# Kernel optimization log

Hardware: AMD Instinct MI355X
Metric: run time of the kernel (lower is better)

The kernel has to match this reference:

```python
import jax, jax.numpy as jnp
import numpy as np

NUM_NODES = 200000
NUM_EDGES = 500000
B = 4096            # batch size (src, dst, neg each B)
ND = 3 * B          # dst nodes of attention block
K = 10              # sampled neighbors per dst
N = ND * (1 + K)    # total tail nodes
D = 128             # dim_embed == dim_node
DE = 128            # dim_edge
DT = 128            # dim_time
H = 2               # num_heads
DIN = 2 * D + DE + DT  # GRUCell input dim


def time_encode(t, w, b):
    # tglite TimeEncode: cos(t * w + b)
    return jnp.cos(t[..., None] * w + b)


def gru_cell(x, h, w_ih, w_hh, b_ih, b_hh):
    # torch.nn.GRUCell, gate order [r, z, n]
    gi = x @ w_ih.T + b_ih
    gh = h @ w_hh.T + b_hh
    i_r, i_z, i_n = jnp.split(gi, 3, axis=-1)
    h_r, h_z, h_n = jnp.split(gh, 3, axis=-1)
    r = jax.nn.sigmoid(i_r + h_r)
    z = jax.nn.sigmoid(i_z + h_z)
    n = jnp.tanh(i_n + r * h_n)
    return (1.0 - z) * n + z * h


def setup_inputs() -> dict:
    key = jax.random.key(0)
    ks = jax.random.split(key, 40)
    p = lambda i, shape: jax.random.normal(ks[i], shape, dtype=jnp.float32) * 0.05
    return {
        "nodes": jax.random.randint(ks[0], (N,), 0, NUM_NODES),
        "eids": jax.random.randint(ks[1], (ND, K), 0, NUM_EDGES),
        "dt_nbr": jax.random.uniform(ks[2], (ND, K), dtype=jnp.float32) * 1000.0,
        "nfeat": p(3, (NUM_NODES, D)),
        "mem_data": p(4, (NUM_NODES, D)),
        "mem_time": jax.random.uniform(ks[5], (NUM_NODES,), dtype=jnp.float32) * 1000.0,
        "mail_data": p(6, (NUM_NODES, 2 * D + DE)),
        "mail_time": jax.random.uniform(ks[7], (NUM_NODES,), dtype=jnp.float32) * 1000.0,
        "efeat": p(8, (NUM_EDGES, DE)),
        "time_w": p(9, (DT,)),
        "time_b": p(10, (DT,)),
        "gru_w_ih": p(11, (3 * D, DIN)),
        "gru_w_hh": p(12, (3 * D, D)),
        "gru_b_ih": p(13, (3 * D,)),
        "gru_b_hh": p(14, (3 * D,)),
        "wq": p(15, (D, D + DT)), "bq": p(16, (D,)),
        "wk": p(17, (D, D + DE + DT)), "bk": p(18, (D,)),
        "wv": p(19, (D, D + DE + DT)), "bv": p(20, (D,)),
        "wo": p(21, (D, 2 * D)), "bo": p(22, (D,)),
        "ln_g": jnp.ones((D,), jnp.float32), "ln_b": jnp.zeros((D,), jnp.float32),
        "ep_sw": p(23, (D, D)), "ep_sb": p(24, (D,)),
        "ep_dw": p(25, (D, D)), "ep_db": p(26, (D,)),
        "ep_ow": p(27, (1, D)), "ep_ob": p(28, (1,)),
    }


def reference(nodes, eids, dt_nbr, nfeat, mem_data, mem_time, mail_data, mail_time,
              efeat, time_w, time_b, gru_w_ih, gru_w_hh, gru_b_ih, gru_b_hh,
              wq, bq, wk, bk, wv, bv, wo, bo, ln_g, ln_b,
              ep_sw, ep_sb, ep_dw, ep_db, ep_ow, ep_ob):
    # ---- update_memory: gather mailbox/memory, time-encode delta, GRUCell ----
    delta = mail_time[nodes] - mem_time[nodes]                  # [N]
    tenc = time_encode(delta, time_w, time_b)                   # [N, DT]
    mail = jnp.concatenate([mail_data[nodes], tenc], axis=1)    # [N, DIN]
    mem = gru_cell(mail, mem_data[nodes], gru_w_ih, gru_w_hh, gru_b_ih, gru_b_hh)  # [N, D]
    # (blk.g.mem.update(nodes, mem, mail_ts) is a persistent-state side effect)

    h = nfeat[nodes] + mem                                      # dst/src hidden states
    dst_h = h[:ND]                                              # [ND, D]
    src_h = h[ND:].reshape(ND, K, D)                            # [ND, K, D]

    # ---- TemporalAttnLayer (TGL-style multi-head attention over neighbors) ----
    zero_tenc = jnp.broadcast_to(jnp.cos(time_b), (ND, DT))     # time_encode(0)
    Q = jnp.concatenate([dst_h, zero_tenc], axis=1) @ wq.T + bq # [ND, D]
    tenc_n = time_encode(dt_nbr, time_w, time_b)                # [ND, K, DT]
    k_in = jnp.concatenate([src_h, efeat[eids], tenc_n], axis=-1)  # [ND, K, D+DE+DT]
    Kf = k_in @ wk.T + bk                                       # [ND, K, D]
    Vf = k_in @ wv.T + bv                                       # [ND, K, D]

    dh = D // H
    Qh = Q.reshape(ND, H, dh)
    Kh = Kf.reshape(ND, K, H, dh)
    Vh = Vf.reshape(ND, K, H, dh)
    att = jax.nn.softmax(jnp.einsum('nhd,nkhd->nkh', Qh, Kh), axis=1)  # [ND, K, H]
    agg = jnp.einsum('nkh,nkhd->nhd', att, Vh).reshape(ND, D)   # [ND, D]

    out = jnp.concatenate([dst_h, agg], axis=1) @ wo.T + bo     # [ND, D]
    out = jax.nn.relu(out)
    mu = out.mean(axis=-1, keepdims=True)
    var = out.var(axis=-1, keepdims=True)
    emb = ln_g * (out - mu) * jax.lax.rsqrt(var + 1e-5) + ln_b  # LayerNorm

    # ---- EdgePredictor over (src, dst) and (src, neg) splits ----
    src_e, dst_e, neg_e = emb[:B], emb[B:2 * B], emb[2 * B:]
    s_proj = src_e @ ep_sw.T + ep_sb
    pos = jax.nn.relu(s_proj + dst_e @ ep_dw.T + ep_db) @ ep_ow.T + ep_ob  # [B, 1]
    neg = jax.nn.relu(s_proj + neg_e @ ep_dw.T + ep_db) @ ep_ow.T + ep_ob  # [B, 1]
    return jnp.concatenate([pos, neg], axis=1)                  # [B, 2]
```

## Files before the change

kernel.cpp:

```cpp
#include <hip/hip_runtime.h>

constexpr int ND_   = 12288;
constexpr int K_    = 10;
constexpr int NTOT  = ND_ * (1 + K_);
constexpr int B_    = 4096;
constexpr int RKV   = ND_ * K_;

constexpr size_t OFF_QB   = 0;
constexpr size_t OFF_AGG  = 786432;
constexpr size_t OFF_HB   = 43253760;
constexpr size_t OFF_KVB  = 51904512;
constexpr size_t OFF_EMB  = 67633152;
constexpr size_t OFF_WCAT = 69206016;
constexpr size_t OFF_WKV  = 69369856;
constexpr size_t OFF_BCAT = 69419008;
constexpr size_t OFF_BKV  = 69419520;
constexpr size_t OFF_WQB  = 69419776;
constexpr size_t OFF_WOB  = 69427968;
constexpr size_t OFF_SWP  = 69444352;
constexpr size_t OFF_DWP  = 69460736;
constexpr size_t OFF_QZ   = 69477120;

#define DEVFN __device__ __forceinline__

typedef __attribute__((ext_vector_type(8))) short bf16x8;
typedef __attribute__((ext_vector_type(4))) short bf16x4;
typedef __attribute__((ext_vector_type(4))) float f32x4;
#define MFMA16(a, b, c) __builtin_amdgcn_mfma_f32_16x16x32_bf16((a), (b), (c), 0, 0, 0)

DEVFN unsigned short f2bf(float x) {
  unsigned int u = __float_as_uint(x);
  u = (u + 0x7FFFu + ((u >> 16) & 1u)) >> 16;
  return (unsigned short)u;
}
DEVFN float bf2f(unsigned short h) { return __uint_as_float(((unsigned int)h) << 16); }

DEVFN float dot4(const float4 a, const float4 b, float acc) {
  acc = fmaf(a.x, b.x, acc);
  acc = fmaf(a.y, b.y, acc);
  acc = fmaf(a.z, b.z, acc);
  acc = fmaf(a.w, b.w, acc);
  return acc;
}
DEVFN float sigmoidf_(float x) { return 1.0f / (1.0f + expf(-x)); }

DEVFN bf16x8 pack8(const float4 a, const float4 b) {
  bf16x8 o;
  o[0] = (short)f2bf(a.x); o[1] = (short)f2bf(a.y);
  o[2] = (short)f2bf(a.z); o[3] = (short)f2bf(a.w);
  o[4] = (short)f2bf(b.x); o[5] = (short)f2bf(b.y);
  o[6] = (short)f2bf(b.z); o[7] = (short)f2bf(b.w);
  return o;
}

__global__ void k0_all(const float* __restrict__ w_ih, const float* __restrict__ w_hh,
                       const float* __restrict__ wk,   const float* __restrict__ wv,
                       const float* __restrict__ wq,   const float* __restrict__ wo,
                       const float* __restrict__ sw,   const float* __restrict__ dwm,
                       const float* __restrict__ b_ih, const float* __restrict__ b_hh,
                       const float* __restrict__ bk,   const float* __restrict__ bv,
                       const float* __restrict__ time_b, const float* __restrict__ bq,
                       unsigned short* __restrict__ WcatP, unsigned short* __restrict__ WkvP,
                       unsigned short* __restrict__ WqB,   unsigned short* __restrict__ WoB,
                       float4* __restrict__ SwP, float4* __restrict__ DwP,
                       float* __restrict__ bcat, float* __restrict__ bkv,
                       float* __restrict__ qzero)
{
  int gid = blockIdx.x * 256 + threadIdx.x;
  if (gid < 327680) {
    int f = gid >> 9, idx = gid & 511;
    int l = idx >> 3, j8 = idx & 7;
    int kt = f >> 5, nt = f & 31;
    int k = kt * 32 + (l >> 4) * 8 + j8;
    int c = nt * 16 + (l & 15);
    int q = c >> 7, jb = (c >> 6) & 1, g = (c >> 4) & 3, j = q * 32 + jb * 16 + (c & 15);
    float w;
    if (g == 0)      w = (k < 512) ? w_ih[(size_t)j * 512 + k]         : w_hh[(size_t)j * 128 + (k - 512)];
    else if (g == 1) w = (k < 512) ? w_ih[(size_t)(128 + j) * 512 + k] : w_hh[(size_t)(128 + j) * 128 + (k - 512)];
    else if (g == 2) w = (k < 512) ? w_ih[(size_t)(256 + j) * 512 + k] : 0.0f;
    else             w = (k < 512) ? 0.0f : w_hh[(size_t)(256 + j) * 128 + (k - 512)];
    WcatP[gid] = f2bf(w);
    return;
  }
  gid -= 327680;
  if (gid < 98304) {
    int f = gid >> 9, idx = gid & 511;
    int l = idx >> 3, j8 = idx & 7;
    int kt = f >> 4, nt = f & 15;
    int k = kt * 32 + (l >> 4) * 8 + j8;
    int c = nt * 16 + (l & 15);
    float w = (c < 128) ? wk[(size_t)c * 384 + k] : wv[(size_t)(c - 128) * 384 + k];
    WkvP[gid] = f2bf(w);
    return;
  }
  gid -= 98304;
  if (gid < 49152) {
    if (gid < 16384) {
      int f = gid >> 9, idx = gid & 511;
      int l = idx >> 3, j8 = idx & 7;
      int kt = f >> 3, nt = f & 7;
      int k = kt * 32 + (l >> 4) * 8 + j8;
      int c = nt * 16 + (l & 15);
      WqB[gid] = f2bf(wq[(size_t)c * 256 + k]);
    } else {
      int g2 = gid - 16384;
      int f = g2 >> 9, idx = g2 & 511;
      int l = idx >> 3, j8 = idx & 7;
      int kt = f >> 3, nt = f & 7;
      int k = kt * 32 + (l >> 4) * 8 + j8;
      int c = nt * 16 + (l & 15);
      WoB[g2] = f2bf(wo[(size_t)c * 256 + k]);
    }
    return;
  }
  gid -= 49152;
  if (gid < 8960) {
    if (gid < 4096) {
      int k4 = gid / 128, c = gid % 128;
      const float* s = sw + c * 128 + 4 * k4;
      SwP[gid] = make_float4(s[0], s[1], s[2], s[3]);
    } else if (gid < 8192) {
      int id = gid - 4096;
      int k4 = id / 128, c = id % 128;
      const float* s = dwm + c * 128 + 4 * k4;
      DwP[id] = make_float4(s[0], s[1], s[2], s[3]);
    } else if (gid < 8704) {
      int id = gid - 8192;
      int q = id >> 7, jb = (id >> 6) & 1, g = (id >> 4) & 3, lcc = id & 15;
      int j = q * 32 + jb * 16 + lcc;
      float b;
      if (g == 0)      b = b_ih[j] + b_hh[j];
      else if (g == 1) b = b_ih[128 + j] + b_hh[128 + j];
      else if (g == 2) b = b_ih[256 + j];
      else             b = b_hh[256 + j];
      bcat[id] = b;
    } else {
      int id = gid - 8704;
      bkv[id] = (id < 128) ? bk[id] : bv[id - 128];
    }
    return;
  }
  gid -= 8960;
  if (gid < 128) {
    float acc = bq[gid];
    for (int k = 0; k < 128; ++k)
      acc = fmaf(cosf(time_b[k]), wq[gid * 256 + 128 + k], acc);
    qzero[gid] = acc;
  }
}

DEVFN float4 k1_gather(int kt, const float* __restrict__ mailp, const float* __restrict__ memp,
                       float drow, const float* __restrict__ time_w,
                       const float* __restrict__ time_b, int sc4) {
  if (kt < 12) return *(const float4*)(mailp + kt * 32 + sc4 * 4);
  if (kt >= 16) return *(const float4*)(memp + (kt - 16) * 32 + sc4 * 4);
  const int c0 = (kt - 12) * 32 + sc4 * 4;
  const float4 w0 = *(const float4*)(time_w + c0);
  const float4 b0 = *(const float4*)(time_b + c0);
  float4 r;
  r.x = cosf(fmaf(drow, w0.x, b0.x)); r.y = cosf(fmaf(drow, w0.y, b0.y));
  r.z = cosf(fmaf(drow, w0.z, b0.z)); r.w = cosf(fmaf(drow, w0.w, b0.w));
  return r;
}
DEVFN void k1_write(unsigned short* __restrict__ buf, int sr, int sc4, float4 v) {
  bf16x4 p;
  p[0] = (short)f2bf(v.x); p[1] = (short)f2bf(v.y);
  p[2] = (short)f2bf(v.z); p[3] = (short)f2bf(v.w);
  *(bf16x4*)(buf + (sr >> 4) * 512 + ((sc4 >> 1) * 16 + (sr & 15)) * 8 + (sc4 & 1) * 4) = p;
}

__global__ __launch_bounds__(256) void k1_fused(
    const int* __restrict__ nodes, const float* __restrict__ mail_data,
    const float* __restrict__ mem_data, const float* __restrict__ mail_time,
    const float* __restrict__ mem_time, const float* __restrict__ time_w,
    const float* __restrict__ time_b, const unsigned short* __restrict__ WcatP,
    const float* __restrict__ bcat, const float* __restrict__ nfeat,
    unsigned short* __restrict__ hb)
{
  __shared__ unsigned short As[2][1024];
  __shared__ int nid[32];
  __shared__ float dd[32];
  const int tid = threadIdx.x;
  const int bid = blockIdx.x;
  const int colb   = (bid >> 3) & 1;
  const int rowblk = (bid & 7) + ((bid >> 4) << 3);
  const int rbase  = rowblk * 32;
  if (tid < 32) {
    int n = nodes[rbase + tid];
    nid[tid] = n;
    dd[tid] = mail_time[n] - mem_time[n];
  }
  __syncthreads();
  const int sr = tid >> 3, sc4 = tid & 7;
  const float* mailp = mail_data + (size_t)nid[sr] * 384;
  const float* memp  = mem_data  + (size_t)nid[sr] * 128;
  const float  drow  = dd[sr];
  const int wn = tid >> 6, l = tid & 63;
  const int lr = l >> 4, lc = l & 15;
  const unsigned short* Bp = WcatP + (size_t)(colb * 16 + wn * 4) * 512 + l * 8;

  f32x4 acc[2][4];
  #pragma unroll
  for (int m = 0; m < 2; ++m)
    #pragma unroll
    for (int bn = 0; bn < 4; ++bn) acc[m][bn] = (f32x4){0.f, 0.f, 0.f, 0.f};

  bf16x8 B[2][4];
  {
    float4 v0 = k1_gather(0, mailp, memp, drow, time_w, time_b, sc4);
    k1_write(As[0], sr, sc4, v0);
    #pragma unroll
    for (int bn = 0; bn < 4; ++bn)
      B[0][bn] = *(const bf16x8*)(Bp + (size_t)bn * 512);
  }
  __syncthreads();

  #pragma unroll
  for (int kt = 0; kt < 20; ++kt) {
    const int cur = kt & 1, nxt = cur ^ 1;
    const bf16x8 A0 = *(const bf16x8*)&As[cur][l * 8];
    const bf16x8 A1 = *(const bf16x8*)&As[cur][512 + l * 8];
    float4 vnext;
    if (kt < 19) {
      vnext = k1_gather(kt + 1, mailp, memp, drow, time_w, time_b, sc4);
      #pragma unroll
      for (int bn = 0; bn < 4; ++bn)
        B[nxt][bn] = *(const bf16x8*)(Bp + ((size_t)(kt + 1) * 32 + bn) * 512);
    }
    #pragma unroll
    for (int bn = 0; bn < 4; ++bn) {
      acc[0][bn] = MFMA16(A0, B[cur][bn], acc[0][bn]);
      acc[1][bn] = MFMA16(A1, B[cur][bn], acc[1][bn]);
    }
    if (kt < 19) k1_write(As[nxt], sr, sc4, vnext);
    __syncthreads();
  }

  const int q = colb * 2 + (wn >> 1), jb = wn & 1;
  float bg[4];
  #pragma unroll
  for (int g = 0; g < 4; ++g) bg[g] = bcat[q * 128 + jb * 64 + g * 16 + lc];
  const int jcol = q * 32 + jb * 16 + lc;

  #pragma unroll
  for (int mt = 0; mt < 2; ++mt) {
    #pragma unroll
    for (int rr = 0; rr < 4; ++rr) {
      const int rloc = mt * 16 + lr * 4 + rr;
      const int grow = rbase + rloc;
      const int n    = nid[rloc];
      const float aR  = acc[mt][0][rr] + bg[0];
      const float aZ  = acc[mt][1][rr] + bg[1];
      const float aNi = acc[mt][2][rr] + bg[2];
      const float aNh = acc[mt][3][rr] + bg[3];
      const float r_  = sigmoidf_(aR);
      const float z_  = sigmoidf_(aZ);
      const float n_  = tanhf(aNi + r_ * aNh);
      const float mem = mem_data[(size_t)n * 128 + jcol];
      const float h = nfeat[(size_t)n * 128 + jcol] + (1.0f - z_) * n_ + z_ * mem;
      hb[(size_t)grow * 128 + jcol] = f2bf(h);
    }
  }
}

DEVFN void k2s(const unsigned short* __restrict__ WkvP, int kt, int wn, int l,
               bf16x8 a, f32x4 (&acc)[4]) {
  #pragma unroll
  for (int bn = 0; bn < 4; ++bn) {
    const bf16x8 b = *(const bf16x8*)(WkvP + ((size_t)(kt * 16 + wn * 4 + bn) * 64 + l) * 8);
    acc[bn] = MFMA16(a, b, acc[bn]);
  }
}

__global__ __launch_bounds__(512) void k2_fused(
    const unsigned short* __restrict__ hb, const int* __restrict__ eids,
    const float* __restrict__ dt_nbr, const float* __restrict__ efeat,
    const float* __restrict__ time_w, const float* __restrict__ time_b,
    const unsigned short* __restrict__ WkvP, const float* __restrict__ bkv,
    unsigned short* __restrict__ KVb)
{
  const int w = threadIdx.x >> 6, l = threadIdx.x & 63;
  const int wm = w >> 2, wn = w & 3;
  const int lr = l >> 4, lc = l & 15;
  const int t16 = blockIdx.x * 2 + wm;
  const int rbase = t16 * 16;

  int eld = 0; float dld = 0.f;
  if (l < 16) { eld = eids[rbase + l]; dld = dt_nbr[rbase + l]; }
  const int   eid = __shfl(eld, lc);
  const float dt  = __shfl(dld, lc);

  const float* ep = efeat + (size_t)eid * 128 + lr * 8;
  bf16x8 ea[4];
  #pragma unroll
  for (int qq = 0; qq < 4; ++qq)
    ea[qq] = pack8(((const float4*)(ep + qq * 32))[0], ((const float4*)(ep + qq * 32))[1]);
  const unsigned short* hp = hb + (size_t)(ND_ + rbase + lc) * 128 + lr * 8;
  bf16x8 hh[4];
  #pragma unroll
  for (int qq = 0; qq < 4; ++qq) hh[qq] = *(const bf16x8*)(hp + qq * 32);
  bf16x8 tt[4];
  #pragma unroll
  for (int qq = 0; qq < 4; ++qq) {
    const int c0 = qq * 32 + lr * 8;
    const float4 w0 = ((const float4*)(time_w + c0))[0];
    const float4 w1 = ((const float4*)(time_w + c0))[1];
    const float4 b0 = ((const float4*)(time_b + c0))[0];
    const float4 b1 = ((const float4*)(time_b + c0))[1];
    float4 u, v;
    u.x = cosf(fmaf(dt, w0.x, b0.x)); u.y = cosf(fmaf(dt, w0.y, b0.y));
    u.z = cosf(fmaf(dt, w0.z, b0.z)); u.w = cosf(fmaf(dt, w0.w, b0.w));
    v.x = cosf(fmaf(dt, w1.x, b1.x)); v.y = cosf(fmaf(dt, w1.y, b1.y));
    v.z = cosf(fmaf(dt, w1.z, b1.z)); v.w = cosf(fmaf(dt, w1.w, b1.w));
    tt[qq] = pack8(u, v);
  }

  f32x4 acc[4];
  #pragma unroll
  for (int bn = 0; bn < 4; ++bn) acc[bn] = (f32x4){0.f, 0.f, 0.f, 0.f};

  #pragma unroll
  for (int qq = 0; qq < 4; ++qq) k2s(WkvP, qq, wn, l, hh[qq], acc);
  #pragma unroll
  for (int qq = 0; qq < 4; ++qq) k2s(WkvP, 4 + qq, wn, l, ea[qq], acc);
  #pragma unroll
  for (int qq = 0; qq < 4; ++qq) k2s(WkvP, 8 + qq, wn, l, tt[qq], acc);

  float bb[4];
  #pragma unroll
  for (int bn = 0; bn < 4; ++bn) bb[bn] = bkv[wn * 64 + bn * 16 + lc];

  #pragma unroll
  for (int rr = 0; rr < 4; ++rr) {
    const size_t grow = (size_t)(rbase + lr * 4 + rr);
    #pragma unroll
    for (int bn = 0; bn < 4; ++bn)
      KVb[grow * 256 + wn * 64 + bn * 16 + lc] = f2bf(acc[bn][rr] + bb[bn]);
  }
}

__global__ __launch_bounds__(512) void kQ_gemm(
    const unsigned short* __restrict__ hb, const unsigned short* __restrict__ WqB,
    const float* __restrict__ qzero, unsigned short* __restrict__ Qb)
{
  const int w = threadIdx.x >> 6, l = threadIdx.x & 63;
  const int wm = w >> 2, wn = w & 3;
  const int lr = l >> 4, lc = l & 15;
  const int t16base = blockIdx.x * 4 + wm * 2;
  const unsigned short* Ar0 = hb + (size_t)(t16base * 16 + lc) * 128 + lr * 8;
  const unsigned short* Ar1 = Ar0 + 16 * 128;

  f32x4 acc[2][2];
  #pragma unroll
  for (int m = 0; m < 2; ++m)
    #pragma unroll
    for (int bn = 0; bn < 2; ++bn) acc[m][bn] = (f32x4){0.f, 0.f, 0.f, 0.f};

  #pragma unroll
  for (int kt = 0; kt < 4; ++kt) {
    const bf16x8 a0 = *(const bf16x8*)(Ar0 + kt * 32);
    const bf16x8 a1 = *(const bf16x8*)(Ar1 + kt * 32);
    #pragma unroll
    for (int bn = 0; bn < 2; ++bn) {
      const bf16x8 b = *(const bf16x8*)(WqB + ((size_t)(kt * 8 + wn * 2 + bn) * 64 + l) * 8);
      acc[0][bn] = MFMA16(a0, b, acc[0][bn]);
      acc[1][bn] = MFMA16(a1, b, acc[1][bn]);
    }
  }

  #pragma unroll
  for (int mt = 0; mt < 2; ++mt)
    #pragma unroll
    for (int rr = 0; rr < 4; ++rr) {
      const int row = (t16base + mt) * 16 + lr * 4 + rr;
      #pragma unroll
      for (int bn = 0; bn < 2; ++bn) {
        const int col = (wn * 2 + bn) * 16 + lc;
        Qb[(size_t)row * 128 + col] = f2bf(acc[mt][bn][rr] + qzero[col]);
      }
    }
}

__global__ __launch_bounds__(256) void kAtt(
    const unsigned short* __restrict__ Qb, const unsigned short* __restrict__ KVb,
    unsigned short* __restrict__ aggb)
{
  const int w = threadIdx.x >> 6, l = threadIdx.x & 63;
  const int i = blockIdx.x * 4 + w;
  const float q0 = bf2f(Qb[(size_t)i * 128 + l]);
  const float q1 = bf2f(Qb[(size_t)i * 128 + 64 + l]);
  const unsigned short* base = KVb + (size_t)i * K_ * 256;

  float s0[K_], s1[K_], v0[K_], v1[K_];
  #pragma unroll
  for (int kk = 0; kk < K_; ++kk) {
    const unsigned short* rp = base + kk * 256;
    const float k0 = bf2f(rp[l]);
    const float k1 = bf2f(rp[64 + l]);
    v0[kk] = bf2f(rp[128 + l]);
    v1[kk] = bf2f(rp[192 + l]);
    float p0 = q0 * k0, p1 = q1 * k1;
    #pragma unroll
    for (int t = 32; t; t >>= 1) { p0 += __shfl_xor(p0, t); p1 += __shfl_xor(p1, t); }
    s0[kk] = p0; s1[kk] = p1;
  }
  float m0 = s0[0], m1 = s1[0];
  #pragma unroll
  for (int kk = 1; kk < K_; ++kk) { m0 = fmaxf(m0, s0[kk]); m1 = fmaxf(m1, s1[kk]); }
  float sum0 = 0.f, sum1 = 0.f, a0 = 0.f, a1 = 0.f;
  #pragma unroll
  for (int kk = 0; kk < K_; ++kk) {
    const float e0 = expf(s0[kk] - m0);
    const float e1 = expf(s1[kk] - m1);
    sum0 += e0; sum1 += e1;
    a0 += e0 * v0[kk]; a1 += e1 * v1[kk];
  }
  aggb[(size_t)i * 128 + l]      = f2bf(a0 / sum0);
  aggb[(size_t)i * 128 + 64 + l] = f2bf(a1 / sum1);
}

__global__ __launch_bounds__(512) void kO_ln(
    const unsigned short* __restrict__ hb, const unsigned short* __restrict__ aggb,
    const unsigned short* __restrict__ WoB, const float* __restrict__ bo,
    const float* __restrict__ ln_g, const float* __restrict__ ln_b,
    float* __restrict__ emb)
{
  __shared__ float ps[64][4], pq[64][4];
  const int w = threadIdx.x >> 6, l = threadIdx.x & 63;
  const int wm = w >> 2, wn = w & 3;
  const int lr = l >> 4, lc = l & 15;
  const int t16base = blockIdx.x * 4 + wm * 2;
  const unsigned short* Ah0 = hb   + (size_t)(t16base * 16 + lc) * 128 + lr * 8;
  const unsigned short* Ah1 = Ah0 + 16 * 128;
  const unsigned short* Ag0 = aggb + (size_t)(t16base * 16 + lc) * 128 + lr * 8;
  const unsigned short* Ag1 = Ag0 + 16 * 128;

  f32x4 acc[2][2];
  #pragma unroll
  for (int m = 0; m < 2; ++m)
    #pragma unroll
    for (int bn = 0; bn < 2; ++bn) acc[m][bn] = (f32x4){0.f, 0.f, 0.f, 0.f};

  #pragma unroll
  for (int kt = 0; kt < 8; ++kt) {
    const bf16x8 a0 = (kt < 4) ? *(const bf16x8*)(Ah0 + kt * 32)
                               : *(const bf16x8*)(Ag0 + (kt - 4) * 32);
    const bf16x8 a1 = (kt < 4) ? *(const bf16x8*)(Ah1 + kt * 32)
                               : *(const bf16x8*)(Ag1 + (kt - 4) * 32);
    #pragma unroll
    for (int bn = 0; bn < 2; ++bn) {
      const bf16x8 b = *(const bf16x8*)(WoB + ((size_t)(kt * 8 + wn * 2 + bn) * 64 + l) * 8);
      acc[0][bn] = MFMA16(a0, b, acc[0][bn]);
      acc[1][bn] = MFMA16(a1, b, acc[1][bn]);
    }
  }

  const int c0 = (wn * 2) * 16 + lc, c1 = c0 + 16;
  const float b0v = bo[c0], b1v = bo[c1];
  float xv0[2][4], xv1[2][4];
  #pragma unroll
  for (int mt = 0; mt < 2; ++mt)
    #pragma unroll
    for (int rr = 0; rr < 4; ++rr) {
      const float x0 = fmaxf(acc[mt][0][rr] + b0v, 0.f);
      const float x1 = fmaxf(acc[mt][1][rr] + b1v, 0.f);
      xv0[mt][rr] = x0; xv1[mt][rr] = x1;
      float s = x0 + x1, q = x0 * x0 + x1 * x1;
      #pragma unroll
      for (int t = 8; t; t >>= 1) { s += __shfl_xor(s, t); q += __shfl_xor(q, t); }
      const int rloc = (wm * 2 + mt) * 16 + lr * 4 + rr;
      if (lc == 0) { ps[rloc][wn] = s; pq[rloc][wn] = q; }
    }
  __syncthreads();
  const float g0 = ln_g[c0], g1 = ln_g[c1], lb0 = ln_b[c0], lb1 = ln_b[c1];
  #pragma unroll
  for (int mt = 0; mt < 2; ++mt)
    #pragma unroll
    for (int rr = 0; rr < 4; ++rr) {
      const int rloc = (wm * 2 + mt) * 16 + lr * 4 + rr;
      const int row  = blockIdx.x * 64 + rloc;
      const float sum = ps[rloc][0] + ps[rloc][1] + ps[rloc][2] + ps[rloc][3];
      const float sq  = pq[rloc][0] + pq[rloc][1] + pq[rloc][2] + pq[rloc][3];
      const float mu  = sum * (1.0f / 128.0f);
      const float var = sq * (1.0f / 128.0f) - mu * mu;
      const float rs  = rsqrtf(var + 1e-5f);
      emb[(size_t)row * 128 + c0] = g0 * (xv0[mt][rr] - mu) * rs + lb0;
      emb[(size_t)row * 128 + c1] = g1 * (xv1[mt][rr] - mu) * rs + lb1;
    }
}

__global__ __launch_bounds__(128) void k3_ep(
    const float* __restrict__ emb, const float4* __restrict__ SwP,
    const float4* __restrict__ DwP, const float* __restrict__ ep_sb,
    const float* __restrict__ ep_db, const float* __restrict__ ep_ow,
    const float* __restrict__ ep_ob, float* __restrict__ out)
{
  __shared__ float se[128], de[128], ne[128];
  __shared__ float redp[2], redn[2];
  const int c = threadIdx.x;
  const int i = blockIdx.x;
  se[c] = emb[(size_t)i * 128 + c];
  de[c] = emb[(size_t)(B_ + i) * 128 + c];
  ne[c] = emb[(size_t)(2 * B_ + i) * 128 + c];
  __syncthreads();
  float sacc = ep_sb[c], dacc = ep_db[c], nacc = ep_db[c];
  for (int k4 = 0; k4 < 32; ++k4) {
    const float4 sw = SwP[k4 * 128 + c];
    const float4 dw = DwP[k4 * 128 + c];
    sacc = dot4(((const float4*)se)[k4], sw, sacc);
    dacc = dot4(((const float4*)de)[k4], dw, dacc);
    nacc = dot4(((const float4*)ne)[k4], dw, nacc);
  }
  const float ow = ep_ow[c];
  float pp = fmaxf(sacc + dacc, 0.f) * ow;
  float pn = fmaxf(sacc + nacc, 0.f) * ow;
  for (int t = 32; t; t >>= 1) { pp += __shfl_xor(pp, t); pn += __shfl_xor(pn, t); }
  if ((c & 63) == 0) { redp[c >> 6] = pp; redn[c >> 6] = pn; }
  __syncthreads();
  if (c == 0) {
    const float ob = ep_ob[0];
    out[i * 2]     = redp[0] + redp[1] + ob;
    out[i * 2 + 1] = redn[0] + redn[1] + ob;
  }
}

extern "C" void kernel_launch(void* const* d_in, const int* in_sizes, int n_in,
                              void* d_out, int out_size, void* d_ws, size_t ws_size,
                              hipStream_t stream) {
  const int*   nodes     = (const int*)d_in[0];
  const int*   eids      = (const int*)d_in[1];
  const float* dt_nbr    = (const float*)d_in[2];
  const float* nfeat     = (const float*)d_in[3];
  const float* mem_data  = (const float*)d_in[4];
  const float* mem_time  = (const float*)d_in[5];
  const float* mail_data = (const float*)d_in[6];
  const float* mail_time = (const float*)d_in[7];
  const float* efeat     = (const float*)d_in[8];
  const float* time_w    = (const float*)d_in[9];
  const float* time_b    = (const float*)d_in[10];
  const float* gru_w_ih  = (const float*)d_in[11];
  const float* gru_w_hh  = (const float*)d_in[12];
  const float* gru_b_ih  = (const float*)d_in[13];
  const float* gru_b_hh  = (const float*)d_in[14];
  const float* wq        = (const float*)d_in[15];
  const float* bq        = (const float*)d_in[16];
  const float* wk        = (const float*)d_in[17];
  const float* bk        = (const float*)d_in[18];
  const float* wv        = (const float*)d_in[19];
  const float* bv        = (const float*)d_in[20];
  const float* wo        = (const float*)d_in[21];
  const float* bo        = (const float*)d_in[22];
  const float* ln_g      = (const float*)d_in[23];
  const float* ln_b      = (const float*)d_in[24];
  const float* ep_sw     = (const float*)d_in[25];
  const float* ep_sb     = (const float*)d_in[26];
  const float* ep_dw     = (const float*)d_in[27];
  const float* ep_db     = (const float*)d_in[28];
  const float* ep_ow     = (const float*)d_in[29];
  const float* ep_ob     = (const float*)d_in[30];
  float* out = (float*)d_out;
  float* ws  = (float*)d_ws;

  unsigned short* Qb    = (unsigned short*)(ws + OFF_QB);
  unsigned short* aggb  = (unsigned short*)(ws + OFF_AGG);
  unsigned short* hb    = (unsigned short*)(ws + OFF_HB);
  unsigned short* KVb   = (unsigned short*)(ws + OFF_KVB);
  float*          emb   = ws + OFF_EMB;
  unsigned short* WcatP = (unsigned short*)(ws + OFF_WCAT);
  unsigned short* WkvP  = (unsigned short*)(ws + OFF_WKV);
  float*          bcat  = ws + OFF_BCAT;
  float*          bkv   = ws + OFF_BKV;
  unsigned short* WqB   = (unsigned short*)(ws + OFF_WQB);
  unsigned short* WoB   = (unsigned short*)(ws + OFF_WOB);
  float4*         SwP   = (float4*)(ws + OFF_SWP);
  float4*         DwP   = (float4*)(ws + OFF_DWP);
  float*          qzero = ws + OFF_QZ;

  k0_all<<<1892, 256, 0, stream>>>(gru_w_ih, gru_w_hh, wk, wv, wq, wo, ep_sw, ep_dw,
                                   gru_b_ih, gru_b_hh, bk, bv, time_b, bq,
                                   WcatP, WkvP, WqB, WoB, SwP, DwP, bcat, bkv, qzero);
  k1_fused<<<(NTOT / 32) * 2, 256, 0, stream>>>(nodes, mail_data, mem_data, mail_time,
                                                mem_time, time_w, time_b, WcatP, bcat,
                                                nfeat, hb);
  k2_fused<<<RKV / 32, 512, 0, stream>>>(hb, eids, dt_nbr, efeat, time_w, time_b,
                                         WkvP, bkv, KVb);
  kQ_gemm<<<ND_ / 64, 512, 0, stream>>>(hb, WqB, qzero, Qb);
  kAtt<<<ND_ / 4, 256, 0, stream>>>(Qb, KVb, aggb);
  kO_ln<<<ND_ / 64, 512, 0, stream>>>(hb, aggb, WoB, bo, ln_g, ln_b, emb);
  k3_ep<<<B_, 128, 0, stream>>>(emb, SwP, DwP, ep_sb, ep_db, ep_ow, ep_ob, out);
}
```

Measured before the change: 444.1 us.

## Load GRU A-fragments directly into registers, drop LDS staging in k1

Restructures the fused GRU kernel so each wave loads its own 16 rows of gathered mail/memory/time-encoding features straight into MFMA A-fragment registers, removing the shared-memory double buffer and per-k-step barriers. Blocks grow to 512 threads covering 64 rows, each wave computing 8 column tiles, and node ids are broadcast with shuffles. It also replaces software float-to-bf16 rounding with the hardware packed convert instruction in k1 and k2. In exchange, B-fragment weight loads are no longer prefetched, more accumulators are held per wave, and each lane now issues wider 32-byte row reads instead of the earlier coalesced pattern.

```diff
diff --git a/kernel.cpp b/kernel.cpp
--- a/kernel.cpp
+++ b/kernel.cpp
@@ -24,7 +24,6 @@
 #define DEVFN __device__ __forceinline__
 
 typedef __attribute__((ext_vector_type(8))) short bf16x8;
-typedef __attribute__((ext_vector_type(4))) short bf16x4;
 typedef __attribute__((ext_vector_type(4))) float f32x4;
 #define MFMA16(a, b, c) __builtin_amdgcn_mfma_f32_16x16x32_bf16((a), (b), (c), 0, 0, 0)
 
@@ -34,6 +33,15 @@
   return (unsigned short)u;
 }
 DEVFN float bf2f(unsigned short h) { return __uint_as_float(((unsigned int)h) << 16); }
+
+DEVFN bf16x8 packcvt(float4 a, float4 b) {
+  union { unsigned int u[4]; bf16x8 v; } r;
+  asm("v_cvt_pk_bf16_f32 %0, %1, %2" : "=v"(r.u[0]) : "v"(a.x), "v"(a.y));
+  asm("v_cvt_pk_bf16_f32 %0, %1, %2" : "=v"(r.u[1]) : "v"(a.z), "v"(a.w));
+  asm("v_cvt_pk_bf16_f32 %0, %1, %2" : "=v"(r.u[2]) : "v"(b.x), "v"(b.y));
+  asm("v_cvt_pk_bf16_f32 %0, %1, %2" : "=v"(r.u[3]) : "v"(b.z), "v"(b.w));
+  return r.v;
+}
 
 DEVFN float dot4(const float4 a, const float4 b, float acc) {
   acc = fmaf(a.x, b.x, acc);
@@ -43,15 +51,6 @@
   return acc;
 }
 DEVFN float sigmoidf_(float x) { return 1.0f / (1.0f + expf(-x)); }
-
-DEVFN bf16x8 pack8(const float4 a, const float4 b) {
-  bf16x8 o;
-  o[0] = (short)f2bf(a.x); o[1] = (short)f2bf(a.y);
-  o[2] = (short)f2bf(a.z); o[3] = (short)f2bf(a.w);
-  o[4] = (short)f2bf(b.x); o[5] = (short)f2bf(b.y);
-  o[6] = (short)f2bf(b.z); o[7] = (short)f2bf(b.w);
-  return o;
-}
 
 __global__ void k0_all(const float* __restrict__ w_ih, const float* __restrict__ w_hh,
                        const float* __restrict__ wk,   const float* __restrict__ wv,
@@ -149,27 +148,29 @@
   }
 }
 
-DEVFN float4 k1_gather(int kt, const float* __restrict__ mailp, const float* __restrict__ memp,
-                       float drow, const float* __restrict__ time_w,
-                       const float* __restrict__ time_b, int sc4) {
-  if (kt < 12) return *(const float4*)(mailp + kt * 32 + sc4 * 4);
-  if (kt >= 16) return *(const float4*)(memp + (kt - 16) * 32 + sc4 * 4);
-  const int c0 = (kt - 12) * 32 + sc4 * 4;
-  const float4 w0 = *(const float4*)(time_w + c0);
-  const float4 b0 = *(const float4*)(time_b + c0);
-  float4 r;
-  r.x = cosf(fmaf(drow, w0.x, b0.x)); r.y = cosf(fmaf(drow, w0.y, b0.y));
-  r.z = cosf(fmaf(drow, w0.z, b0.z)); r.w = cosf(fmaf(drow, w0.w, b0.w));
-  return r;
-}
-DEVFN void k1_write(unsigned short* __restrict__ buf, int sr, int sc4, float4 v) {
-  bf16x4 p;
-  p[0] = (short)f2bf(v.x); p[1] = (short)f2bf(v.y);
-  p[2] = (short)f2bf(v.z); p[3] = (short)f2bf(v.w);
-  *(bf16x4*)(buf + (sr >> 4) * 512 + ((sc4 >> 1) * 16 + (sr & 15)) * 8 + (sc4 & 1) * 4) = p;
-}
-
-__global__ __launch_bounds__(256) void k1_fused(
+DEVFN void k1_ld(int kt, const float* __restrict__ mailp, const float* __restrict__ memp,
+                 float drow, const float* __restrict__ time_w, const float* __restrict__ time_b,
+                 int lr, float4& v0, float4& v1) {
+  if (kt < 12) {
+    v0 = *(const float4*)(mailp + kt * 32);
+    v1 = *(const float4*)(mailp + kt * 32 + 4);
+  } else if (kt >= 16) {
+    v0 = *(const float4*)(memp + (kt - 16) * 32);
+    v1 = *(const float4*)(memp + (kt - 16) * 32 + 4);
+  } else {
+    const int c0 = (kt - 12) * 32 + lr * 8;
+    const float4 w0 = *(const float4*)(time_w + c0);
+    const float4 w1 = *(const float4*)(time_w + c0 + 4);
+    const float4 b0 = *(const float4*)(time_b + c0);
+    const float4 b1 = *(const float4*)(time_b + c0 + 4);
+    v0.x = cosf(fmaf(drow, w0.x, b0.x)); v0.y = cosf(fmaf(drow, w0.y, b0.y));
+    v0.z = cosf(fmaf(drow, w0.z, b0.z)); v0.w = cosf(fmaf(drow, w0.w, b0.w));
+    v1.x = cosf(fmaf(drow, w1.x, b1.x)); v1.y = cosf(fmaf(drow, w1.y, b1.y));
+    v1.z = cosf(fmaf(drow, w1.z, b1.z)); v1.w = cosf(fmaf(drow, w1.w, b1.w));
+  }
+}
+
+__global__ __launch_bounds__(512) void k1_fused(
     const int* __restrict__ nodes, const float* __restrict__ mail_data,
     const float* __restrict__ mem_data, const float* __restrict__ mail_time,
     const float* __restrict__ mem_time, const float* __restrict__ time_w,
@@ -177,87 +178,67 @@
     const float* __restrict__ bcat, const float* __restrict__ nfeat,
     unsigned short* __restrict__ hb)
 {
-  __shared__ unsigned short As[2][1024];
-  __shared__ int nid[32];
-  __shared__ float dd[32];
   const int tid = threadIdx.x;
   const int bid = blockIdx.x;
   const int colb   = (bid >> 3) & 1;
   const int rowblk = (bid & 7) + ((bid >> 4) << 3);
-  const int rbase  = rowblk * 32;
-  if (tid < 32) {
-    int n = nodes[rbase + tid];
-    nid[tid] = n;
-    dd[tid] = mail_time[n] - mem_time[n];
-  }
-  __syncthreads();
-  const int sr = tid >> 3, sc4 = tid & 7;
-  const float* mailp = mail_data + (size_t)nid[sr] * 384;
-  const float* memp  = mem_data  + (size_t)nid[sr] * 128;
-  const float  drow  = dd[sr];
-  const int wn = tid >> 6, l = tid & 63;
+  const int w = tid >> 6, l = tid & 63;
+  const int wm = w >> 1, wn = w & 1;
   const int lr = l >> 4, lc = l & 15;
-  const unsigned short* Bp = WcatP + (size_t)(colb * 16 + wn * 4) * 512 + l * 8;
-
-  f32x4 acc[2][4];
-  #pragma unroll
-  for (int m = 0; m < 2; ++m)
-    #pragma unroll
-    for (int bn = 0; bn < 4; ++bn) acc[m][bn] = (f32x4){0.f, 0.f, 0.f, 0.f};
-
-  bf16x8 B[2][4];
-  {
-    float4 v0 = k1_gather(0, mailp, memp, drow, time_w, time_b, sc4);
-    k1_write(As[0], sr, sc4, v0);
-    #pragma unroll
-    for (int bn = 0; bn < 4; ++bn)
-      B[0][bn] = *(const bf16x8*)(Bp + (size_t)bn * 512);
-  }
-  __syncthreads();
-
+  const int rbase = rowblk * 64 + wm * 16;
+
+  int nld = 0; float dld = 0.f;
+  if (l < 16) {
+    nld = nodes[rbase + l];
+    dld = mail_time[nld] - mem_time[nld];
+  }
+  const int   nrow = __shfl(nld, lc);
+  const float drow = __shfl(dld, lc);
+  const float* mailp = mail_data + (size_t)nrow * 384 + lr * 8;
+  const float* memp  = mem_data  + (size_t)nrow * 128 + lr * 8;
+
+  const int q = colb * 2 + wn;
+  const unsigned short* Bp = WcatP + (size_t)(q * 8) * 512 + l * 8;
+
+  f32x4 acc[8];
+  #pragma unroll
+  for (int bn = 0; bn < 8; ++bn) acc[bn] = (f32x4){0.f, 0.f, 0.f, 0.f};
+
+  float4 c0v, c1v, n0v, n1v;
+  k1_ld(0, mailp, memp, drow, time_w, time_b, lr, c0v, c1v);
   #pragma unroll
   for (int kt = 0; kt < 20; ++kt) {
-    const int cur = kt & 1, nxt = cur ^ 1;
-    const bf16x8 A0 = *(const bf16x8*)&As[cur][l * 8];
-    const bf16x8 A1 = *(const bf16x8*)&As[cur][512 + l * 8];
-    float4 vnext;
-    if (kt < 19) {
-      vnext = k1_gather(kt + 1, mailp, memp, drow, time_w, time_b, sc4);
-      #pragma unroll
-      for (int bn = 0; bn < 4; ++bn)
-        B[nxt][bn] = *(const bf16x8*)(Bp + ((size_t)(kt + 1) * 32 + bn) * 512);
-    }
-    #pragma unroll
-    for (int bn = 0; bn < 4; ++bn) {
-      acc[0][bn] = MFMA16(A0, B[cur][bn], acc[0][bn]);
-      acc[1][bn] = MFMA16(A1, B[cur][bn], acc[1][bn]);
-    }
-    if (kt < 19) k1_write(As[nxt], sr, sc4, vnext);
-    __syncthreads();
-  }
-
-  const int q = colb * 2 + (wn >> 1), jb = wn & 1;
-  float bg[4];
-  #pragma unroll
-  for (int g = 0; g < 4; ++g) bg[g] = bcat[q * 128 + jb * 64 + g * 16 + lc];
-  const int jcol = q * 32 + jb * 16 + lc;
-
-  #pragma unroll
-  for (int mt = 0; mt < 2; ++mt) {
-    #pragma unroll
-    for (int rr = 0; rr < 4; ++rr) {
-      const int rloc = mt * 16 + lr * 4 + rr;
-      const int grow = rbase + rloc;
-      const int n    = nid[rloc];
-      const float aR  = acc[mt][0][rr] + bg[0];
-      const float aZ  = acc[mt][1][rr] + bg[1];
-      const float aNi = acc[mt][2][rr] + bg[2];
-      const float aNh = acc[mt][3][rr] + bg[3];
+    if (kt < 19) k1_ld(kt + 1, mailp, memp, drow, time_w, time_b, lr, n0v, n1v);
+    const bf16x8 A = packcvt(c0v, c1v);
+    #pragma unroll
+    for (int bn = 0; bn < 8; ++bn) {
+      const bf16x8 Bf = *(const bf16x8*)(Bp + ((size_t)kt * 32 + bn) * 512);
+      acc[bn] = MFMA16(A, Bf, acc[bn]);
+    }
+    c0v = n0v; c1v = n1v;
+  }
+
+  float bg[8];
+  #pragma unroll
+  for (int bn = 0; bn < 8; ++bn) bg[bn] = bcat[q * 128 + bn * 16 + lc];
+
+  #pragma unroll
+  for (int rr = 0; rr < 4; ++rr) {
+    const int rloc = lr * 4 + rr;
+    const int grow = rbase + rloc;
+    const int n2   = __shfl(nld, rloc);
+    #pragma unroll
+    for (int jb = 0; jb < 2; ++jb) {
+      const int jcol = q * 32 + jb * 16 + lc;
+      const float aR  = acc[jb * 4 + 0][rr] + bg[jb * 4 + 0];
+      const float aZ  = acc[jb * 4 + 1][rr] + bg[jb * 4 + 1];
+      const float aNi = acc[jb * 4 + 2][rr] + bg[jb * 4 + 2];
+      const float aNh = acc[jb * 4 + 3][rr] + bg[jb * 4 + 3];
       const float r_  = sigmoidf_(aR);
       const float z_  = sigmoidf_(aZ);
       const float n_  = tanhf(aNi + r_ * aNh);
-      const float mem = mem_data[(size_t)n * 128 + jcol];
-      const float h = nfeat[(size_t)n * 128 + jcol] + (1.0f - z_) * n_ + z_ * mem;
+      const float mem = mem_data[(size_t)n2 * 128 + jcol];
+      const float h = nfeat[(size_t)n2 * 128 + jcol] + (1.0f - z_) * n_ + z_ * mem;
       hb[(size_t)grow * 128 + jcol] = f2bf(h);
     }
   }
@@ -294,7 +275,7 @@
   bf16x8 ea[4];
   #pragma unroll
   for (int qq = 0; qq < 4; ++qq)
-    ea[qq] = pack8(((const float4*)(ep + qq * 32))[0], ((const float4*)(ep + qq * 32))[1]);
+    ea[qq] = packcvt(((const float4*)(ep + qq * 32))[0], ((const float4*)(ep + qq * 32))[1]);
   const unsigned short* hp = hb + (size_t)(ND_ + rbase + lc) * 128 + lr * 8;
   bf16x8 hh[4];
   #pragma unroll
@@ -312,7 +293,7 @@
     u.z = cosf(fmaf(dt, w0.z, b0.z)); u.w = cosf(fmaf(dt, w0.w, b0.w));
     v.x = cosf(fmaf(dt, w1.x, b1.x)); v.y = cosf(fmaf(dt, w1.y, b1.y));
     v.z = cosf(fmaf(dt, w1.z, b1.z)); v.w = cosf(fmaf(dt, w1.w, b1.w));
-    tt[qq] = pack8(u, v);
+    tt[qq] = packcvt(u, v);
   }
 
   f32x4 acc[4];
@@ -579,7 +560,7 @@
   k0_all<<<1892, 256, 0, stream>>>(gru_w_ih, gru_w_hh, wk, wv, wq, wo, ep_sw, ep_dw,
                                    gru_b_ih, gru_b_hh, bk, bv, time_b, bq,
                                    WcatP, WkvP, WqB, WoB, SwP, DwP, bcat, bkv, qzero);
-  k1_fused<<<(NTOT / 32) * 2, 256, 0, stream>>>(nodes, mail_data, mem_data, mail_time,
+  k1_fused<<<(NTOT / 64) * 2, 512, 0, stream>>>(nodes, mail_data, mem_data, mail_time,
                                                 mem_time, time_w, time_b, WcatP, bcat,
                                                 nfeat, hb);
   k2_fused<<<RKV / 32, 512, 0, stream>>>(hb, eids, dt_nbr, efeat, time_w, time_b,
```

New measurement: 595.4 us. +34.1%, slower.
